# Performance work log

Hardware: AMD Instinct MI355X
Metric: run time of the kernel (lower is better)

Reference implementation:

```python
import jax, jax.numpy as jnp
import numpy as np

BATCH = 262144

def _f64_bits_msb_first(val):
    # IEEE754 double bit pattern, MSB first (equivalent to struct.pack('>d', val))
    u = int(np.frombuffer(np.float64(val).tobytes(), dtype=np.uint64)[0])
    return [float((u >> (63 - i)) & 1) for i in range(64)]

def setup_inputs() -> dict:
    key = jax.random.key(0)
    # Table T[j] = bits of 2^(j/64), shape [64 entries, 64 bits]
    table = np.array([_f64_bits_msb_first(2.0 ** (j / 64.0)) for j in range(64)],
                     dtype=np.float32)
    idx_bits = jax.random.randint(key, (BATCH, 6), 0, 2).astype(jnp.int32)
    return {"table_bits": jnp.asarray(table), "idx_bits": idx_bits}

def reference(table_bits, idx_bits):
    """Fused MUX-tree table lookup.

    Each MUXGate(sel, B, A) = sel ? B : A on binary pulses. Level k selects on
    idx_bits[..., k] (MSB first) between the lower and upper half of the
    surviving table entries, exactly reproducing the 6-level tree of 64-bit MUXes.
    """
    batch_shape = idx_bits.shape[:-1]
    # [B, 64 entries, 64 bits]
    x = jnp.broadcast_to(table_bits, batch_shape + table_bits.shape)
    for k in range(6):  # b5 (weight 32) down to b0 (weight 1)
        n = x.shape[-2] // 2
        sel = (idx_bits[..., k] > 0)[..., None, None]
        x = jnp.where(sel, x[..., n:, :], x[..., :n, :])
    return x[..., 0, :]  # [B, 64] bit pulses of 2^(idx/64)
```

## Files before the change

### kernel.cpp

```cpp
#include <hip/hip_runtime.h>


#define ROWS 256

typedef float nfloat4 __attribute__((ext_vector_type(4)));

__global__ __launch_bounds__(256) void
spike_lut_kernel(const float* __restrict__ table,
                 const int* __restrict__ idx_bits,
                 nfloat4* __restrict__ out4,
                 int batch) {
    __shared__ unsigned long long s_mask[64];
    __shared__ int s_idx[ROWS];

    const int  tid  = threadIdx.x;
    const int  wave = tid >> 6;
    const int  lane = tid & 63;
    const long b0   = (long)blockIdx.x * ROWS;
    const bool full = (b0 + ROWS) <= batch;

    #pragma unroll
    for (int i = 0; i < 16; ++i) {
        const int row = wave * 16 + i;
        const float f = table[row * 64 + lane];
        const unsigned long long m = __ballot(f > 0.5f);
        if (lane == 0) s_mask[row] = m;
    }

    {
        int idx = 0;
        const long b = b0 + tid;
        if (b < (long)batch) {
            const int* p = idx_bits + b * 6;
            #pragma unroll
            for (int k = 0; k < 6; ++k)
                idx = (idx << 1) | (p[k] > 0 ? 1 : 0);
        }
        s_idx[tid] = idx;
    }
    __syncthreads();

    if (full) {
        #pragma unroll
        for (int it = 0; it < 16; ++it) {
            const int g  = it * 256 + tid;
            const int bl = g >> 4;
            const int q  = g & 15;
            const unsigned int r = (unsigned int)(s_mask[s_idx[bl]] >> (q * 4));
            nfloat4 v;
            v.x = (r & 1u) ? 1.0f : 0.0f;
            v.y = (r & 2u) ? 1.0f : 0.0f;
            v.z = (r & 4u) ? 1.0f : 0.0f;
            v.w = (r & 8u) ? 1.0f : 0.0f;
            __builtin_nontemporal_store(v, &out4[(b0 + bl) * 16 + q]);
        }
    } else {
        #pragma unroll
        for (int it = 0; it < 16; ++it) {
            const int g  = it * 256 + tid;
            const int bl = g >> 4;
            const int q  = g & 15;
            if (b0 + bl < batch) {
                const unsigned int r = (unsigned int)(s_mask[s_idx[bl]] >> (q * 4));
                nfloat4 v;
                v.x = (r & 1u) ? 1.0f : 0.0f;
                v.y = (r & 2u) ? 1.0f : 0.0f;
                v.z = (r & 4u) ? 1.0f : 0.0f;
                v.w = (r & 8u) ? 1.0f : 0.0f;
                __builtin_nontemporal_store(v, &out4[(b0 + bl) * 16 + q]);
            }
        }
    }
}

extern "C" void kernel_launch(void* const* d_in, const int* in_sizes, int n_in,
                              void* d_out, int out_size, void* d_ws, size_t ws_size,
                              hipStream_t stream) {
    const float* table    = (const float*)d_in[0];
    const int*   idx_bits = (const int*)d_in[1];
    nfloat4*     out4     = (nfloat4*)d_out;

    const int batch  = in_sizes[1] / 6;
    const int blocks = (batch + ROWS - 1) / ROWS;

    spike_lut_kernel<<<blocks, 256, 0, stream>>>(table, idx_bits, out4, batch);
}
```

Measured before the change: 87.51 us.

## Split mask build into separate kernel and use one thread per output float4

Moves the table-to-bitmask ballot into a tiny one-block kernel that writes 64 masks to workspace. The main kernel now maps one thread per output float4, each recomputing its row index from six global loads and reading the mask from global memory, with no shared memory or barrier. This removes the per-block table reload and syncthreads, but adds a second launch, 16x redundant idx loads per row, and plain stores instead of nontemporal ones.

Result: slower. 91.27 us (+4.3%).

```diff
diff --git a/kernel.cpp b/kernel.cpp
--- a/kernel.cpp
+++ b/kernel.cpp
@@ -1,76 +1,47 @@
 #include <hip/hip_runtime.h>
 
-
-#define ROWS 256
 
 typedef float nfloat4 __attribute__((ext_vector_type(4)));
 
 __global__ __launch_bounds__(256) void
-spike_lut_kernel(const float* __restrict__ table,
-                 const int* __restrict__ idx_bits,
-                 nfloat4* __restrict__ out4,
-                 int batch) {
-    __shared__ unsigned long long s_mask[64];
-    __shared__ int s_idx[ROWS];
-
-    const int  tid  = threadIdx.x;
-    const int  wave = tid >> 6;
-    const int  lane = tid & 63;
-    const long b0   = (long)blockIdx.x * ROWS;
-    const bool full = (b0 + ROWS) <= batch;
-
+make_masks_kernel(const float* __restrict__ table,
+                  unsigned long long* __restrict__ masks) {
+    const int wave = threadIdx.x >> 6;
+    const int lane = threadIdx.x & 63;
     #pragma unroll
     for (int i = 0; i < 16; ++i) {
         const int row = wave * 16 + i;
         const float f = table[row * 64 + lane];
         const unsigned long long m = __ballot(f > 0.5f);
-        if (lane == 0) s_mask[row] = m;
+        if (lane == 0) masks[row] = m;
     }
+}
 
-    {
-        int idx = 0;
-        const long b = b0 + tid;
-        if (b < (long)batch) {
-            const int* p = idx_bits + b * 6;
-            #pragma unroll
-            for (int k = 0; k < 6; ++k)
-                idx = (idx << 1) | (p[k] > 0 ? 1 : 0);
-        }
-        s_idx[tid] = idx;
-    }
-    __syncthreads();
+__global__ __launch_bounds__(256) void
+spike_lut_kernel(const unsigned long long* __restrict__ masks,
+                 const int* __restrict__ idx_bits,
+                 nfloat4* __restrict__ out4,
+                 long n4) {
+    const long g = (long)blockIdx.x * 256 + threadIdx.x;
+    if (g >= n4) return;
 
-    if (full) {
-        #pragma unroll
-        for (int it = 0; it < 16; ++it) {
-            const int g  = it * 256 + tid;
-            const int bl = g >> 4;
-            const int q  = g & 15;
-            const unsigned int r = (unsigned int)(s_mask[s_idx[bl]] >> (q * 4));
-            nfloat4 v;
-            v.x = (r & 1u) ? 1.0f : 0.0f;
-            v.y = (r & 2u) ? 1.0f : 0.0f;
-            v.z = (r & 4u) ? 1.0f : 0.0f;
-            v.w = (r & 8u) ? 1.0f : 0.0f;
-            __builtin_nontemporal_store(v, &out4[(b0 + bl) * 16 + q]);
-        }
-    } else {
-        #pragma unroll
-        for (int it = 0; it < 16; ++it) {
-            const int g  = it * 256 + tid;
-            const int bl = g >> 4;
-            const int q  = g & 15;
-            if (b0 + bl < batch) {
-                const unsigned int r = (unsigned int)(s_mask[s_idx[bl]] >> (q * 4));
-                nfloat4 v;
-                v.x = (r & 1u) ? 1.0f : 0.0f;
-                v.y = (r & 2u) ? 1.0f : 0.0f;
-                v.z = (r & 4u) ? 1.0f : 0.0f;
-                v.w = (r & 8u) ? 1.0f : 0.0f;
-                __builtin_nontemporal_store(v, &out4[(b0 + bl) * 16 + q]);
-            }
-        }
-    }
+    const long b = g >> 4;
+    const int  q = (int)(g & 15);
+
+    const int* p = idx_bits + b * 6;
+    int idx = 0;
+    #pragma unroll
+    for (int k = 0; k < 6; ++k)
+        idx = (idx << 1) | (p[k] > 0 ? 1 : 0);
+
+    const unsigned int r = (unsigned int)(masks[idx] >> (q * 4));
+
+    nfloat4 v;
+    v.x = (r & 1u) ? 1.0f : 0.0f;
+    v.y = (r & 2u) ? 1.0f : 0.0f;
+    v.z = (r & 4u) ? 1.0f : 0.0f;
+    v.w = (r & 8u) ? 1.0f : 0.0f;
+    out4[g] = v;
 }
 
 extern "C" void kernel_launch(void* const* d_in, const int* in_sizes, int n_in,
@@ -79,9 +50,12 @@
     const float* table    = (const float*)d_in[0];
     const int*   idx_bits = (const int*)d_in[1];
     nfloat4*     out4     = (nfloat4*)d_out;
+    unsigned long long* masks = (unsigned long long*)d_ws;
 
-    const int batch  = in_sizes[1] / 6;
-    const int blocks = (batch + ROWS - 1) / ROWS;
+    const int  batch = in_sizes[1] / 6;
+    const long n4    = (long)batch * 16;
+    const int  blocks = (int)((n4 + 255) / 256);
 
-    spike_lut_kernel<<<blocks, 256, 0, stream>>>(table, idx_bits, out4, batch);
+    make_masks_kernel<<<1, 256, 0, stream>>>(table, masks);
+    spike_lut_kernel<<<blocks, 256, 0, stream>>>(masks, idx_bits, out4, n4);
 }
```
